# Kernel tuning notes

Measured on AMD Instinct MI355X. Metric: run time of the kernel, lower is better.

Reference implementation:

```python
import jax, jax.numpy as jnp
import numpy as np

N_NODES = 100000
N_EDGES = 1600000
IN_DIM = 128
HID_DIM = 32
OUT_DIM = 64
N_REL = 8
N_CLASSES = 2


def setup_inputs() -> dict:
    key = jax.random.key(0)
    ks = jax.random.split(key, 12)
    x = jax.random.normal(ks[0], (N_NODES, IN_DIM), dtype=jnp.float32)
    edge_index = jax.random.randint(ks[1], (2, N_EDGES), 0, N_NODES, dtype=jnp.int64)
    edge_type = jax.random.randint(ks[2], (N_EDGES,), 0, N_REL, dtype=jnp.int64)
    # FastRGCNConv params: per-relation weight W [R, in, out], root weight, bias
    def glorot(k, shape):
        fan_in, fan_out = shape[-2], shape[-1]
        s = jnp.sqrt(6.0 / (fan_in + fan_out))
        return jax.random.uniform(k, shape, jnp.float32, -s, s)
    W1 = glorot(ks[3], (N_REL, IN_DIM, HID_DIM))
    root1 = glorot(ks[4], (IN_DIM, HID_DIM))
    b1 = jnp.zeros((HID_DIM,), jnp.float32)
    W2 = glorot(ks[5], (N_REL, HID_DIM, OUT_DIM))
    root2 = glorot(ks[6], (HID_DIM, OUT_DIM))
    b2 = jnp.zeros((OUT_DIM,), jnp.float32)
    lin_w = glorot(ks[7], (OUT_DIM, N_CLASSES))
    lin_b = jnp.zeros((N_CLASSES,), jnp.float32)
    return {"x": x, "edge_index": edge_index, "edge_type": edge_type,
            "W1": W1, "root1": root1, "b1": b1,
            "W2": W2, "root2": root2, "b2": b2,
            "lin_w": lin_w, "lin_b": lin_b}


def _fast_rgcn_conv(x, W, root, b, src, dst, etype, n_nodes):
    """FastRGCNConv: per-relation transform, gather by (src, relation),
    mean-aggregate by destination, plus root transform and bias."""
    # Transform all nodes by all relation weights: [N, R, H]
    xW = jnp.einsum('nf,rfh->nrh', x, W)
    # Per-edge message: relation-specific transformed source feature [E, H]
    msg = xW[src, etype]
    agg = jax.ops.segment_sum(msg, dst, num_segments=n_nodes)
    deg = jax.ops.segment_sum(jnp.ones((src.shape[0],), x.dtype), dst,
                              num_segments=n_nodes)
    agg = agg / jnp.maximum(deg, 1.0)[:, None]  # mean aggregation
    return agg + x @ root + b


def reference(x, edge_index, edge_type, W1, root1, b1, W2, root2, b2, lin_w, lin_b):
    src, dst = edge_index[0], edge_index[1]
    n = x.shape[0]
    h = jax.nn.relu(_fast_rgcn_conv(x, W1, root1, b1, src, dst, edge_type, n))
    h = _fast_rgcn_conv(h, W2, root2, b2, src, dst, edge_type, n)
    return h @ lin_w + lin_b
```

## Files before the change

### kernel.cpp

```cpp
#include <hip/hip_runtime.h>

#define NN      100000
#define IN_DIM  128
#define HID     32
#define ODIM    64
#define L1C     288
#define L2K     288
#define NWGS    196
#define NCB     784
#define CCAP    40
#define RECCAP  2304
#define G2ST    296
#define PKCAP   512

using bf16x8 = __attribute__((ext_vector_type(8))) short;
using f32x4  = __attribute__((ext_vector_type(4))) float;

__device__ __forceinline__ float bf2f(short s) {
    unsigned int u = ((unsigned int)(unsigned short)s) << 16;
    float f; __builtin_memcpy(&f, &u, 4); return f;
}
__device__ __forceinline__ short f2bf(float f) {
    unsigned int u; __builtin_memcpy(&u, &f, 4);
    u += 0x7fffu + ((u >> 16) & 1u);
    return (short)(u >> 16);
}
__device__ __forceinline__ float ldf(const void* p, int i, int f32) {
    return f32 ? ((const float*)p)[i] : bf2f(((const short*)p)[i]);
}
__device__ __forceinline__ int ldi(const int* p, long long i, int i64) {
    return i64 ? p[2 * i] : p[(int)i];
}

__global__ __launch_bounds__(1024) void detect(const short* __restrict__ x,
                                               const short* __restrict__ W1,
                                               const short* __restrict__ r1,
                                               const short* __restrict__ W2,
                                               const short* __restrict__ r2,
                                               const short* __restrict__ lw,
                                               const int* __restrict__ ei,
                                               const int* __restrict__ et,
                                               int* __restrict__ flags) {
    __shared__ int cnt[8];
    if (threadIdx.x < 8) cnt[threadIdx.x] = 0;
    __syncthreads();
    const short* ptrs[6] = {x, W1, r1, W2, r2, lw};
    const int    nsmp[6] = {1024, 1024, 1024, 1024, 1024, 64};
    int t = threadIdx.x;
#pragma unroll
    for (int j = 0; j < 6; ++j) {
        if (t < nsmp[j]) {
            unsigned int s = (unsigned short)ptrs[j][2 * t];
            unsigned int e = (s >> 7) & 0xFF;
            if (e >= 140u || (e >= 1u && e <= 100u)) atomicAdd(&cnt[j], 1);
        }
    }
    if (t < 128) {
        if (ei[2 * t + 1] != 0) atomicAdd(&cnt[6], 1);
        if (et[2 * t + 1] != 0) atomicAdd(&cnt[7], 1);
    }
    __syncthreads();
    if (t == 0) {
        const int ns[6] = {1024, 1024, 1024, 1024, 1024, 64};
        for (int j = 0; j < 6; ++j) flags[j] = (cnt[j] * 4 > ns[j]) ? 1 : 0;
        flags[6] = (cnt[6] == 0) ? 1 : 0;
        flags[7] = (cnt[7] == 0) ? 1 : 0;
    }
}

__global__ __launch_bounds__(256) void prep_all(const void* __restrict__ W1,
                                                const void* __restrict__ root1,
                                                const void* __restrict__ W2,
                                                const void* __restrict__ root2,
                                                const short* __restrict__ b1,
                                                const short* __restrict__ b2,
                                                const void* __restrict__ lin_w,
                                                const short* __restrict__ lin_b,
                                                short* __restrict__ w1t,
                                                short* __restrict__ w2ct,
                                                short* __restrict__ smallc,
                                                int* __restrict__ cbTot,
                                                const int* __restrict__ flags) {
    if (blockIdx.x == 0) {
        for (int j = threadIdx.x; j < NCB; j += 256) cbTot[j] = 0;
    }
    int gi = blockIdx.x * 256 + threadIdx.x;
    if (gi < L1C * IN_DIM) {
        int c = gi >> 7, f = gi & 127;
        float v;
        if (c < 256) { int r = c >> 5, h = c & 31; v = ldf(W1, (r * IN_DIM + f) * HID + h, flags[1]); }
        else         { v = ldf(root1, f * HID + (c - 256), flags[2]); }
        w1t[c * IN_DIM + f] = f2bf(v);
        return;
    }
    int i2 = gi - L1C * IN_DIM;
    if (i2 < ODIM * L2K) {
        int c = i2 / L2K, k = i2 % L2K;
        float v;
        if (k < 256) { int r = k >> 5, kk = k & 31; v = ldf(W2, (r * HID + kk) * ODIM + c, flags[3]); }
        else         { v = ldf(root2, (k - 256) * ODIM + c, flags[4]); }
        w2ct[c * L2K + k] = f2bf(v);
        return;
    }
    int i3 = i2 - ODIM * L2K;
    if (i3 < 256) {
        if (i3 < 32)        smallc[i3] = b1[i3];
        else if (i3 < 96)   smallc[i3] = b2[i3 - 32];
        else if (i3 < 224)  smallc[i3] = f2bf(ldf(lin_w, i3 - 96, flags[5]));
        else if (i3 < 226)  smallc[i3] = lin_b[i3 - 224];
    }
}

__global__ __launch_bounds__(1024) void scatter_coarse(const int* __restrict__ ei,
                                                       const int* __restrict__ et,
                                                       int* __restrict__ cnt,
                                                       int* __restrict__ cbTot,
                                                       int* __restrict__ seg, int E,
                                                       const int* __restrict__ flags) {
    __shared__ int cur[NCB];
    if (threadIdx.x < NCB) cur[threadIdx.x] = 0;
    __syncthreads();
    int i64 = flags[6], t64 = flags[7];
    int epw = (E + NWGS - 1) / NWGS;
    int lo = blockIdx.x * epw;
    int hi = lo + epw; if (hi > E) hi = E;
    for (int i = lo + threadIdx.x; i < hi; i += 1024) {
        int s = ldi(ei, i, i64);
        int d = ldi(ei, (long long)E + i, i64);
        int r = ldi(et, i, t64);
        int cb = d >> 7;
        int pos = atomicAdd(&cur[cb], 1);
        if (pos < CCAP)
            seg[(cb * NWGS + (int)blockIdx.x) * CCAP + pos] = ((d & 127) << 20) | (s << 3) | r;
    }
    __syncthreads();
    if (threadIdx.x < NCB) {
        int c = cur[threadIdx.x];
        c = c < CCAP ? c : CCAP;
        cnt[blockIdx.x * NCB + threadIdx.x] = c;
        atomicAdd(&cbTot[threadIdx.x], c);
    }
}

__global__ __launch_bounds__(256) void build_cb(const int* __restrict__ cnt,
                                                const int* __restrict__ seg,
                                                const int* __restrict__ cbTot,
                                                int* __restrict__ off,
                                                float* __restrict__ inv_deg,
                                                int* __restrict__ packed) {
    __shared__ int cntl[NWGS], soff[NWGS];
    __shared__ int recs[RECCAP];
    __shared__ int deg8[1024], base8[1024], kcur8[1024];
    __shared__ int stmp[256];
    __shared__ int gbase_s;
    int cb = blockIdx.x, tid = threadIdx.x;
    {
        int part = 0;
        for (int j = tid; j < cb; j += 256) part += cbTot[j];
        stmp[tid] = part; __syncthreads();
        for (int o = 128; o > 0; o >>= 1) {
            if (tid < o) stmp[tid] += stmp[tid + o];
            __syncthreads();
        }
        if (tid == 0) gbase_s = stmp[0];
        __syncthreads();
    }
    if (tid < NWGS) cntl[tid] = cnt[tid * NCB + cb];
#pragma unroll
    for (int j = 0; j < 4; ++j) { deg8[tid + j * 256] = 0; kcur8[tid + j * 256] = 0; }
    __syncthreads();
    int v = (tid < NWGS) ? cntl[tid] : 0;
    stmp[tid] = v; __syncthreads();
    for (int o = 1; o < 256; o <<= 1) {
        int u = (tid >= o) ? stmp[tid - o] : 0;
        __syncthreads();
        stmp[tid] += u;
        __syncthreads();
    }
    if (tid < NWGS) soff[tid] = stmp[tid] - v;
    int tot = stmp[255]; if (tot > RECCAP) tot = RECCAP;
    __syncthreads();
    int wave = tid >> 6, lane = tid & 63;
    for (int g = wave; g < NWGS; g += 4) {
        int c = cntl[g], b = soff[g];
        const int* sp = seg + (cb * NWGS + g) * CCAP;
        for (int e = lane; e < c; e += 64)
            if (b + e < RECCAP) recs[b + e] = sp[e];
    }
    __syncthreads();
    for (int i = tid; i < tot; i += 256) {
        int rec = recs[i];
        atomicAdd(&deg8[((rec >> 20) << 3) | (rec & 7)], 1);
    }
    __syncthreads();
    int k0 = tid * 4;
    int d0 = deg8[k0], d1 = deg8[k0 + 1], d2 = deg8[k0 + 2], d3 = deg8[k0 + 3];
    int s01 = d0 + d1, sum4 = s01 + d2 + d3;
    stmp[tid] = sum4; __syncthreads();
    for (int o = 1; o < 256; o <<= 1) {
        int u = (tid >= o) ? stmp[tid - o] : 0;
        __syncthreads();
        stmp[tid] += u;
        __syncthreads();
    }
    int excl = stmp[tid] - sum4;
    base8[k0] = excl; base8[k0 + 1] = excl + d0;
    base8[k0 + 2] = excl + s01; base8[k0 + 3] = excl + s01 + d2;
    __syncthreads();
    int gbase = gbase_s;
    if (tid < 128) {
        int b0 = base8[tid * 8];
        int b1 = (tid < 127) ? base8[(tid + 1) * 8] : tot;
        int dv = b1 - b0;
        int node = cb * 128 + tid;
        if (node <= NN) {
            off[node] = gbase + b0;
            if (node < NN) inv_deg[node] = 1.0f / (float)(dv > 1 ? dv : 1);
        }
    }
    __syncthreads();
    for (int i = tid; i < tot; i += 256) {
        int rec = recs[i];
        int key = ((rec >> 20) << 3) | (rec & 7);
        int p = atomicAdd(&kcur8[key], 1);
        packed[gbase + base8[key] + p] = (((rec >> 20) & 15) << 24) | (rec & 0xFFFFF);
    }
}

__global__ __launch_bounds__(256) void gemm1(const void* __restrict__ x,
                                             const short* __restrict__ w1t,
                                             short* __restrict__ xw,
                                             const int* __restrict__ flags) {
    int wave = threadIdx.x >> 6, lane = threadIdx.x & 63;
    int m = lane & 15, quad = lane >> 4;
    int row0 = (blockIdx.x * 4 + wave) * 64;
    if (row0 >= NN) return;

    bf16x8 a[4][4];
    int fp32 = flags[0];
#pragma unroll
    for (int t = 0; t < 4; ++t) {
        int row = row0 + t * 16 + m;
        int rc = row < NN ? row : NN - 1;
        if (fp32) {
            const float* xr = (const float*)x + rc * IN_DIM + quad * 8;
#pragma unroll
            for (int kt = 0; kt < 4; ++kt) {
                const f32x4* q = (const f32x4*)(xr + kt * 32);
                f32x4 u0 = q[0], u1 = q[1];
                bf16x8 tt;
                tt[0] = f2bf(u0[0]); tt[1] = f2bf(u0[1]); tt[2] = f2bf(u0[2]); tt[3] = f2bf(u0[3]);
                tt[4] = f2bf(u1[0]); tt[5] = f2bf(u1[1]); tt[6] = f2bf(u1[2]); tt[7] = f2bf(u1[3]);
                a[t][kt] = tt;
            }
        } else {
            const short* xr = (const short*)x + rc * IN_DIM + quad * 8;
#pragma unroll
            for (int kt = 0; kt < 4; ++kt) a[t][kt] = *(const bf16x8*)(xr + kt * 32);
        }
    }

    for (int ct = 0; ct < 18; ++ct) {
        const short* wp = w1t + (ct * 16 + m) * IN_DIM + quad * 8;
        bf16x8 b[4];
#pragma unroll
        for (int kt = 0; kt < 4; ++kt) b[kt] = *(const bf16x8*)(wp + kt * 32);
#pragma unroll
        for (int t = 0; t < 4; ++t) {
            f32x4 acc = {0.f, 0.f, 0.f, 0.f};
#pragma unroll
            for (int kt = 0; kt < 4; ++kt)
                acc = __builtin_amdgcn_mfma_f32_16x16x32_bf16(a[t][kt], b[kt], acc, 0, 0, 0);
#pragma unroll
            for (int i = 0; i < 4; ++i) {
                int r = row0 + t * 16 + quad * 4 + i;
                if (r < NN) xw[r * L1C + ct * 16 + m] = f2bf(acc[i]);
            }
        }
    }
}

__global__ __launch_bounds__(256) void agg1(const short* __restrict__ xw,
                                            const int* __restrict__ off,
                                            const int* __restrict__ packed,
                                            const float* __restrict__ inv_deg,
                                            const short* __restrict__ smallc,
                                            short* __restrict__ h) {
    __shared__ int pk_l[PKCAP];
    __shared__ float invl[16];
    int tid = threadIdx.x;
    int row0 = blockIdx.x * 16;
    if (tid < 16) invl[tid] = inv_deg[row0 + tid];
    int st = off[row0];
    int tot = off[row0 + 16] - st;
    for (int j = tid; j < tot && j < PKCAP; j += 256) pk_l[j] = packed[st + j];
    __syncthreads();

    int node = tid >> 4, l = tid & 15;
    int s = off[row0 + node] - st, en = off[row0 + node + 1] - st;
    const short* xp = xw + l * 2;
    float a0 = 0.f, a1 = 0.f;

    auto ldpk = [&](int j) -> int {
        return (j < PKCAP) ? pk_l[j] : packed[st + j];
    };
    auto gv = [&](int pk) -> unsigned {
        return *(const unsigned*)(xp + ((pk >> 3) & 0x1FFFF) * L1C + (pk & 7) * 32);
    };

    int i = s;
    for (; i + 7 < en; i += 8) {
        int p0 = ldpk(i),     p1 = ldpk(i + 1), p2 = ldpk(i + 2), p3 = ldpk(i + 3);
        int p4 = ldpk(i + 4), p5 = ldpk(i + 5), p6 = ldpk(i + 6), p7 = ldpk(i + 7);
        unsigned v0 = gv(p0), v1 = gv(p1), v2 = gv(p2), v3 = gv(p3);
        unsigned v4 = gv(p4), v5 = gv(p5), v6 = gv(p6), v7 = gv(p7);
        a0 += ((bf2f((short)(v0 & 0xFFFF)) + bf2f((short)(v1 & 0xFFFF)))
             + (bf2f((short)(v2 & 0xFFFF)) + bf2f((short)(v3 & 0xFFFF))))
            + ((bf2f((short)(v4 & 0xFFFF)) + bf2f((short)(v5 & 0xFFFF)))
             + (bf2f((short)(v6 & 0xFFFF)) + bf2f((short)(v7 & 0xFFFF))));
        a1 += ((bf2f((short)(v0 >> 16)) + bf2f((short)(v1 >> 16)))
             + (bf2f((short)(v2 >> 16)) + bf2f((short)(v3 >> 16))))
            + ((bf2f((short)(v4 >> 16)) + bf2f((short)(v5 >> 16)))
             + (bf2f((short)(v6 >> 16)) + bf2f((short)(v7 >> 16))));
    }
    for (; i + 3 < en; i += 4) {
        int p0 = ldpk(i), p1 = ldpk(i + 1), p2 = ldpk(i + 2), p3 = ldpk(i + 3);
        unsigned v0 = gv(p0), v1 = gv(p1), v2 = gv(p2), v3 = gv(p3);
        a0 += (bf2f((short)(v0 & 0xFFFF)) + bf2f((short)(v1 & 0xFFFF)))
            + (bf2f((short)(v2 & 0xFFFF)) + bf2f((short)(v3 & 0xFFFF)));
        a1 += (bf2f((short)(v0 >> 16)) + bf2f((short)(v1 >> 16)))
            + (bf2f((short)(v2 >> 16)) + bf2f((short)(v3 >> 16)));
    }
    for (; i < en; ++i) {
        unsigned v = gv(ldpk(i));
        a0 += bf2f((short)(v & 0xFFFF));
        a1 += bf2f((short)(v >> 16));
    }

    float inv = invl[node];
    unsigned rt = *(const unsigned*)(xw + (row0 + node) * L1C + 256 + l * 2);
    unsigned bc = *(const unsigned*)(smallc + l * 2);
    float o0 = a0 * inv + bf2f((short)(rt & 0xFFFF)) + bf2f((short)(bc & 0xFFFF));
    float o1 = a1 * inv + bf2f((short)(rt >> 16)) + bf2f((short)(bc >> 16));
    o0 = o0 > 0.f ? o0 : 0.f;
    o1 = o1 > 0.f ? o1 : 0.f;
    unsigned w = ((unsigned)(unsigned short)f2bf(o1) << 16) | (unsigned short)f2bf(o0);
    *(unsigned*)(h + (row0 + node) * HID + l * 2) = w;
}

__global__ __launch_bounds__(256) void agg2_fused(const short* __restrict__ h,
                                                  const int* __restrict__ off,
                                                  const int* __restrict__ packed,
                                                  const float* __restrict__ inv_deg,
                                                  const short* __restrict__ w2ct,
                                                  const short* __restrict__ smallc,
                                                  float* __restrict__ out) {
    __shared__ __align__(16) short g2l[16 * G2ST];
    __shared__ int pk_l[PKCAP];
    __shared__ float red[4][16][2];
    __shared__ float invl[16];
    int tid = threadIdx.x;
    int row0 = blockIdx.x * 16;
    if (tid < 16) invl[tid] = inv_deg[row0 + tid];
    int st = off[row0];
    int tot = off[row0 + 16] - st;
    {
        unsigned* gz = (unsigned*)g2l;
        const int nu = 16 * G2ST / 2;
        for (int j = tid; j < nu; j += 256) gz[j] = 0;
        for (int j = tid; j < tot && j < PKCAP; j += 256) pk_l[j] = packed[st + j];
    }
    __syncthreads();

    int node = tid >> 4, l = tid & 15;
    int s = off[row0 + node] - st, en = off[row0 + node + 1] - st;
    float inv = invl[node];
    const short* hp = h + l * 2;
    short* grow = g2l + node * G2ST + l * 2;
    float a0 = 0.f, a1 = 0.f;
    int cur = -1;

    auto ldpk = [&](int j) -> int {
        return (j < PKCAP) ? pk_l[j] : packed[st + j];
    };
    auto acc_edge = [&](int pk, unsigned hv) {
        int rel = pk & 7;
        bool nr = (rel != cur);
        float lo = bf2f((short)(hv & 0xFFFF)) * inv;
        float hi = bf2f((short)(hv >> 16)) * inv;
        a0 = (nr ? 0.f : a0) + lo;
        a1 = (nr ? 0.f : a1) + hi;
        cur = rel;
        unsigned w = ((unsigned)(unsigned short)f2bf(a1) << 16)
                   | (unsigned short)f2bf(a0);
        *(unsigned*)(grow + rel * 32) = w;
    };

    int i = s;
    for (; i + 7 < en; i += 8) {
        int p0 = ldpk(i),     p1 = ldpk(i + 1), p2 = ldpk(i + 2), p3 = ldpk(i + 3);
        int p4 = ldpk(i + 4), p5 = ldpk(i + 5), p6 = ldpk(i + 6), p7 = ldpk(i + 7);
        unsigned v0 = *(const unsigned*)(hp + ((p0 >> 3) & 0x1FFFF) * HID);
        unsigned v1 = *(const unsigned*)(hp + ((p1 >> 3) & 0x1FFFF) * HID);
        unsigned v2 = *(const unsigned*)(hp + ((p2 >> 3) & 0x1FFFF) * HID);
        unsigned v3 = *(const unsigned*)(hp + ((p3 >> 3) & 0x1FFFF) * HID);
        unsigned v4 = *(const unsigned*)(hp + ((p4 >> 3) & 0x1FFFF) * HID);
        unsigned v5 = *(const unsigned*)(hp + ((p5 >> 3) & 0x1FFFF) * HID);
        unsigned v6 = *(const unsigned*)(hp + ((p6 >> 3) & 0x1FFFF) * HID);
        unsigned v7 = *(const unsigned*)(hp + ((p7 >> 3) & 0x1FFFF) * HID);
        acc_edge(p0, v0); acc_edge(p1, v1); acc_edge(p2, v2); acc_edge(p3, v3);
        acc_edge(p4, v4); acc_edge(p5, v5); acc_edge(p6, v6); acc_edge(p7, v7);
    }
    for (; i + 3 < en; i += 4) {
        int p0 = ldpk(i), p1 = ldpk(i + 1), p2 = ldpk(i + 2), p3 = ldpk(i + 3);
        unsigned v0 = *(const unsigned*)(hp + ((p0 >> 3) & 0x1FFFF) * HID);
        unsigned v1 = *(const unsigned*)(hp + ((p1 >> 3) & 0x1FFFF) * HID);
        unsigned v2 = *(const unsigned*)(hp + ((p2 >> 3) & 0x1FFFF) * HID);
        unsigned v3 = *(const unsigned*)(hp + ((p3 >> 3) & 0x1FFFF) * HID);
        acc_edge(p0, v0); acc_edge(p1, v1); acc_edge(p2, v2); acc_edge(p3, v3);
    }
    for (; i < en; ++i) {
        int p = ldpk(i);
        unsigned v = *(const unsigned*)(hp + ((p >> 3) & 0x1FFFF) * HID);
        acc_edge(p, v);
    }

    *(unsigned*)(grow + 256) = *(const unsigned*)(h + (row0 + node) * HID + l * 2);
    __syncthreads();

    int wave = tid >> 6, lane = tid & 63;
    int m15 = lane & 15, quad = lane >> 4;
    const short* wp = w2ct + (wave * 16 + m15) * L2K + quad * 8;
    bf16x8 a[9], b[9];
#pragma unroll
    for (int kt = 0; kt < 9; ++kt) {
        b[kt] = *(const bf16x8*)(wp + kt * 32);
        a[kt] = *(const bf16x8*)(&g2l[m15 * G2ST + quad * 8 + kt * 32]);
    }
    f32x4 acc = {0.f, 0.f, 0.f, 0.f};
#pragma unroll
    for (int kt = 0; kt < 9; ++kt)
        acc = __builtin_amdgcn_mfma_f32_16x16x32_bf16(a[kt], b[kt], acc, 0, 0, 0);

    int c = wave * 16 + m15;
    float lw0 = bf2f(smallc[96 + c * 2 + 0]);
    float lw1 = bf2f(smallc[96 + c * 2 + 1]);
    float b2c = bf2f(smallc[32 + c]);
    float pr0[4], pr1[4];
#pragma unroll
    for (int i2 = 0; i2 < 4; ++i2) {
        float v = acc[i2] + b2c;
        pr0[i2] = v * lw0;
        pr1[i2] = v * lw1;
    }
#pragma unroll
    for (int o = 1; o < 16; o <<= 1) {
#pragma unroll
        for (int i2 = 0; i2 < 4; ++i2) {
            pr0[i2] += __shfl_xor(pr0[i2], o, 64);
            pr1[i2] += __shfl_xor(pr1[i2], o, 64);
        }
    }
    if (m15 == 0) {
#pragma unroll
        for (int i2 = 0; i2 < 4; ++i2) {
            red[wave][quad * 4 + i2][0] = pr0[i2];
            red[wave][quad * 4 + i2][1] = pr1[i2];
        }
    }
    __syncthreads();
    if (tid < 32) {
        int row = tid >> 1, j = tid & 1;
        float v = red[0][row][j] + red[1][row][j] + red[2][row][j] + red[3][row][j]
                + bf2f(smallc[224 + j]);
        out[(row0 + row) * 2 + j] = v;
    }
}

extern "C" void kernel_launch(void* const* d_in, const int* in_sizes, int n_in,
                              void* d_out, int out_size, void* d_ws, size_t ws_size,
                              hipStream_t stream) {
    const void* x     = d_in[0];
    const int*  ei    = (const int*)d_in[1];
    const int*  etype = (const int*)d_in[2];
    const void* W1    = d_in[3];
    const void* root1 = d_in[4];
    const void* b1    = d_in[5];
    const void* W2    = d_in[6];
    const void* root2 = d_in[7];
    const void* b2    = d_in[8];
    const void* lin_w = d_in[9];
    const void* lin_b = d_in[10];
    float* out = (float*)d_out;

    const int E = in_sizes[2];

    char* p = (char*)d_ws;
    auto alloc = [&](size_t bytes) { char* r = p; p += (bytes + 255) & ~(size_t)255; return (void*)r; };
    int*   flags   = (int*)  alloc(256);
    int*   off     = (int*)  alloc((size_t)(NN + 1) * 4);
    float* inv_deg = (float*)alloc((size_t)NN * 4);
    int*   packed  = (int*)  alloc((size_t)E * 4);
    int*   cnt     = (int*)  alloc((size_t)NWGS * NCB * 4);
    int*   cbTot   = (int*)  alloc((size_t)NCB * 4);
    int*   seg     = (int*)  alloc((size_t)NCB * NWGS * CCAP * 4);
    short* w1t     = (short*)alloc((size_t)L1C * IN_DIM * 2);
    short* w2ct    = (short*)alloc((size_t)ODIM * L2K * 2);
    short* smallc  = (short*)alloc(256 * 2);
    short* h       = (short*)alloc((size_t)NN * HID * 2);
    short* xw1     = (short*)alloc((size_t)NN * L1C * 2);

    detect<<<1, 1024, 0, stream>>>((const short*)x, (const short*)W1, (const short*)root1,
                                   (const short*)W2, (const short*)root2, (const short*)lin_w,
                                   ei, etype, flags);
    const int prep_items = L1C * IN_DIM + ODIM * L2K + 256;
    prep_all<<<(prep_items + 255) / 256, 256, 0, stream>>>(W1, root1, W2, root2,
                                                           (const short*)b1, (const short*)b2,
                                                           lin_w, (const short*)lin_b,
                                                           w1t, w2ct, smallc, cbTot, flags);

    scatter_coarse<<<NWGS, 1024, 0, stream>>>(ei, etype, cnt, cbTot, seg, E, flags);
    build_cb<<<NCB, 256, 0, stream>>>(cnt, seg, cbTot, off, inv_deg, packed);

    gemm1<<<((NN + 63) / 64 + 3) / 4, 256, 0, stream>>>(x, w1t, xw1, flags);
    agg1<<<NN / 16, 256, 0, stream>>>(xw1, off, packed, inv_deg, smallc, h);
    agg2_fused<<<NN / 16, 256, 0, stream>>>(h, off, packed, inv_deg, w2ct, smallc, out);
}
```

Baseline: 280.3 us.

## Aggregate raw features per relation before layer-1 GEMM and fuse into one kernel

Result: slower. 335.9 us (+19.8%).

```diff
diff --git a/kernel.cpp b/kernel.cpp
--- a/kernel.cpp
+++ b/kernel.cpp
@@ -5,12 +5,14 @@
 #define HID     32
 #define ODIM    64
 #define L1C     288
+#define L1K     1152
 #define L2K     288
 #define NWGS    196
 #define NCB     784
 #define CCAP    40
 #define RECCAP  2304
 #define G2ST    296
+#define SST     1160
 #define PKCAP   512
 
 using bf16x8 = __attribute__((ext_vector_type(8))) short;
@@ -76,7 +78,7 @@
                                                 const short* __restrict__ b2,
                                                 const void* __restrict__ lin_w,
                                                 const short* __restrict__ lin_b,
-                                                short* __restrict__ w1t,
+                                                short* __restrict__ w1tn,
                                                 short* __restrict__ w2ct,
                                                 short* __restrict__ smallc,
                                                 int* __restrict__ cbTot,
@@ -85,15 +87,15 @@
         for (int j = threadIdx.x; j < NCB; j += 256) cbTot[j] = 0;
     }
     int gi = blockIdx.x * 256 + threadIdx.x;
-    if (gi < L1C * IN_DIM) {
-        int c = gi >> 7, f = gi & 127;
+    if (gi < HID * L1K) {
+        int c = gi / L1K, k = gi - c * L1K;
         float v;
-        if (c < 256) { int r = c >> 5, h = c & 31; v = ldf(W1, (r * IN_DIM + f) * HID + h, flags[1]); }
-        else         { v = ldf(root1, f * HID + (c - 256), flags[2]); }
-        w1t[c * IN_DIM + f] = f2bf(v);
+        if (k < 1024) { int r = k >> 7, f = k & 127; v = ldf(W1, (r * IN_DIM + f) * HID + c, flags[1]); }
+        else          { v = ldf(root1, (k - 1024) * HID + c, flags[2]); }
+        w1tn[c * L1K + k] = f2bf(v);
         return;
     }
-    int i2 = gi - L1C * IN_DIM;
+    int i2 = gi - HID * L1K;
     if (i2 < ODIM * L2K) {
         int c = i2 / L2K, k = i2 % L2K;
         float v;
@@ -108,6 +110,22 @@
         else if (i3 < 96)   smallc[i3] = b2[i3 - 32];
         else if (i3 < 224)  smallc[i3] = f2bf(ldf(lin_w, i3 - 96, flags[5]));
         else if (i3 < 226)  smallc[i3] = lin_b[i3 - 224];
+    }
+}
+
+__global__ __launch_bounds__(256) void xcast(const void* __restrict__ x,
+                                             short* __restrict__ xb,
+                                             const int* __restrict__ flags) {
+    int gi = blockIdx.x * 256 + threadIdx.x;
+    if (flags[0]) {
+        const f32x4* q = (const f32x4*)x + gi * 2;
+        f32x4 u0 = q[0], u1 = q[1];
+        bf16x8 t;
+        t[0] = f2bf(u0[0]); t[1] = f2bf(u0[1]); t[2] = f2bf(u0[2]); t[3] = f2bf(u0[3]);
+        t[4] = f2bf(u1[0]); t[5] = f2bf(u1[1]); t[6] = f2bf(u1[2]); t[7] = f2bf(u1[3]);
+        ((bf16x8*)xb)[gi] = t;
+    } else {
+        ((bf16x8*)xb)[gi] = ((const bf16x8*)x)[gi];
     }
 }
 
@@ -227,125 +245,100 @@
     }
 }
 
-__global__ __launch_bounds__(256) void gemm1(const void* __restrict__ x,
-                                             const short* __restrict__ w1t,
-                                             short* __restrict__ xw,
-                                             const int* __restrict__ flags) {
-    int wave = threadIdx.x >> 6, lane = threadIdx.x & 63;
-    int m = lane & 15, quad = lane >> 4;
-    int row0 = (blockIdx.x * 4 + wave) * 64;
-    if (row0 >= NN) return;
-
-    bf16x8 a[4][4];
-    int fp32 = flags[0];
-#pragma unroll
-    for (int t = 0; t < 4; ++t) {
-        int row = row0 + t * 16 + m;
-        int rc = row < NN ? row : NN - 1;
-        if (fp32) {
-            const float* xr = (const float*)x + rc * IN_DIM + quad * 8;
-#pragma unroll
-            for (int kt = 0; kt < 4; ++kt) {
-                const f32x4* q = (const f32x4*)(xr + kt * 32);
-                f32x4 u0 = q[0], u1 = q[1];
-                bf16x8 tt;
-                tt[0] = f2bf(u0[0]); tt[1] = f2bf(u0[1]); tt[2] = f2bf(u0[2]); tt[3] = f2bf(u0[3]);
-                tt[4] = f2bf(u1[0]); tt[5] = f2bf(u1[1]); tt[6] = f2bf(u1[2]); tt[7] = f2bf(u1[3]);
-                a[t][kt] = tt;
-            }
-        } else {
-            const short* xr = (const short*)x + rc * IN_DIM + quad * 8;
-#pragma unroll
-            for (int kt = 0; kt < 4; ++kt) a[t][kt] = *(const bf16x8*)(xr + kt * 32);
-        }
-    }
-
-    for (int ct = 0; ct < 18; ++ct) {
-        const short* wp = w1t + (ct * 16 + m) * IN_DIM + quad * 8;
-        bf16x8 b[4];
-#pragma unroll
-        for (int kt = 0; kt < 4; ++kt) b[kt] = *(const bf16x8*)(wp + kt * 32);
-#pragma unroll
-        for (int t = 0; t < 4; ++t) {
-            f32x4 acc = {0.f, 0.f, 0.f, 0.f};
-#pragma unroll
-            for (int kt = 0; kt < 4; ++kt)
-                acc = __builtin_amdgcn_mfma_f32_16x16x32_bf16(a[t][kt], b[kt], acc, 0, 0, 0);
-#pragma unroll
-            for (int i = 0; i < 4; ++i) {
-                int r = row0 + t * 16 + quad * 4 + i;
-                if (r < NN) xw[r * L1C + ct * 16 + m] = f2bf(acc[i]);
-            }
-        }
-    }
-}
-
-__global__ __launch_bounds__(256) void agg1(const short* __restrict__ xw,
-                                            const int* __restrict__ off,
-                                            const int* __restrict__ packed,
-                                            const float* __restrict__ inv_deg,
-                                            const short* __restrict__ smallc,
-                                            short* __restrict__ h) {
-    __shared__ int pk_l[PKCAP];
+__global__ __launch_bounds__(256) void agg_gemm1(const short* __restrict__ xb,
+                                                 const int* __restrict__ off,
+                                                 const int* __restrict__ packed,
+                                                 const float* __restrict__ inv_deg,
+                                                 const short* __restrict__ w1tn,
+                                                 const short* __restrict__ smallc,
+                                                 short* __restrict__ h) {
+    __shared__ __align__(16) short S[16 * SST];
+    __shared__ __align__(16) int pk_l[PKCAP];
     __shared__ float invl[16];
+    float* red2 = (float*)pk_l;
     int tid = threadIdx.x;
     int row0 = blockIdx.x * 16;
     if (tid < 16) invl[tid] = inv_deg[row0 + tid];
     int st = off[row0];
     int tot = off[row0 + 16] - st;
-    for (int j = tid; j < tot && j < PKCAP; j += 256) pk_l[j] = packed[st + j];
+    {
+        uint4 z = {0, 0, 0, 0};
+        uint4* sz = (uint4*)S;
+        for (int j = tid; j < 16 * SST / 8; j += 256) sz[j] = z;
+        for (int j = tid; j < tot && j < PKCAP; j += 256) pk_l[j] = packed[st + j];
+    }
     __syncthreads();
 
     int node = tid >> 4, l = tid & 15;
     int s = off[row0 + node] - st, en = off[row0 + node + 1] - st;
-    const short* xp = xw + l * 2;
-    float a0 = 0.f, a1 = 0.f;
-
-    auto ldpk = [&](int j) -> int {
-        return (j < PKCAP) ? pk_l[j] : packed[st + j];
+    float inv = invl[node];
+    const short* xp = xb + l * 8;
+    short* Sp = S + node * SST + l * 8;
+    float ac[8] = {0.f, 0.f, 0.f, 0.f, 0.f, 0.f, 0.f, 0.f};
+    int cur = -1;
+
+    auto acc_edge = [&](int pk, bf16x8 v) {
+        int rel = pk & 7;
+        bool nr = (rel != cur);
+        bf16x8 wv;
+#pragma unroll
+        for (int d = 0; d < 8; ++d) {
+            float xv = bf2f(v[d]);
+            ac[d] = (nr ? 0.f : ac[d]) + xv * inv;
+            wv[d] = f2bf(ac[d]);
+        }
+        cur = rel;
+        *(bf16x8*)(Sp + rel * 128) = wv;
     };
-    auto gv = [&](int pk) -> unsigned {
-        return *(const unsigned*)(xp + ((pk >> 3) & 0x1FFFF) * L1C + (pk & 7) * 32);
+    auto run = [&](auto LD) {
+        int i = s;
+        for (; i + 3 < en; i += 4) {
+            int p0 = LD(i), p1 = LD(i + 1), p2 = LD(i + 2), p3 = LD(i + 3);
+            bf16x8 v0 = *(const bf16x8*)(xp + ((p0 >> 3) & 0x1FFFF) * IN_DIM);
+            bf16x8 v1 = *(const bf16x8*)(xp + ((p1 >> 3) & 0x1FFFF) * IN_DIM);
+            bf16x8 v2 = *(const bf16x8*)(xp + ((p2 >> 3) & 0x1FFFF) * IN_DIM);
+            bf16x8 v3 = *(const bf16x8*)(xp + ((p3 >> 3) & 0x1FFFF) * IN_DIM);
+            acc_edge(p0, v0); acc_edge(p1, v1); acc_edge(p2, v2); acc_edge(p3, v3);
+        }
+        for (; i < en; ++i) {
+            int p = LD(i);
+            bf16x8 v = *(const bf16x8*)(xp + ((p >> 3) & 0x1FFFF) * IN_DIM);
+            acc_edge(p, v);
+        }
     };
-
-    int i = s;
-    for (; i + 7 < en; i += 8) {
-        int p0 = ldpk(i),     p1 = ldpk(i + 1), p2 = ldpk(i + 2), p3 = ldpk(i + 3);
-        int p4 = ldpk(i + 4), p5 = ldpk(i + 5), p6 = ldpk(i + 6), p7 = ldpk(i + 7);
-        unsigned v0 = gv(p0), v1 = gv(p1), v2 = gv(p2), v3 = gv(p3);
-        unsigned v4 = gv(p4), v5 = gv(p5), v6 = gv(p6), v7 = gv(p7);
-        a0 += ((bf2f((short)(v0 & 0xFFFF)) + bf2f((short)(v1 & 0xFFFF)))
-             + (bf2f((short)(v2 & 0xFFFF)) + bf2f((short)(v3 & 0xFFFF))))
-            + ((bf2f((short)(v4 & 0xFFFF)) + bf2f((short)(v5 & 0xFFFF)))
-             + (bf2f((short)(v6 & 0xFFFF)) + bf2f((short)(v7 & 0xFFFF))));
-        a1 += ((bf2f((short)(v0 >> 16)) + bf2f((short)(v1 >> 16)))
-             + (bf2f((short)(v2 >> 16)) + bf2f((short)(v3 >> 16))))
-            + ((bf2f((short)(v4 >> 16)) + bf2f((short)(v5 >> 16)))
-             + (bf2f((short)(v6 >> 16)) + bf2f((short)(v7 >> 16))));
-    }
-    for (; i + 3 < en; i += 4) {
-        int p0 = ldpk(i), p1 = ldpk(i + 1), p2 = ldpk(i + 2), p3 = ldpk(i + 3);
-        unsigned v0 = gv(p0), v1 = gv(p1), v2 = gv(p2), v3 = gv(p3);
-        a0 += (bf2f((short)(v0 & 0xFFFF)) + bf2f((short)(v1 & 0xFFFF)))
-            + (bf2f((short)(v2 & 0xFFFF)) + bf2f((short)(v3 & 0xFFFF)));
-        a1 += (bf2f((short)(v0 >> 16)) + bf2f((short)(v1 >> 16)))
-            + (bf2f((short)(v2 >> 16)) + bf2f((short)(v3 >> 16)));
-    }
-    for (; i < en; ++i) {
-        unsigned v = gv(ldpk(i));
-        a0 += bf2f((short)(v & 0xFFFF));
-        a1 += bf2f((short)(v >> 16));
-    }
-
-    float inv = invl[node];
-    unsigned rt = *(const unsigned*)(xw + (row0 + node) * L1C + 256 + l * 2);
-    unsigned bc = *(const unsigned*)(smallc + l * 2);
-    float o0 = a0 * inv + bf2f((short)(rt & 0xFFFF)) + bf2f((short)(bc & 0xFFFF));
-    float o1 = a1 * inv + bf2f((short)(rt >> 16)) + bf2f((short)(bc >> 16));
-    o0 = o0 > 0.f ? o0 : 0.f;
-    o1 = o1 > 0.f ? o1 : 0.f;
-    unsigned w = ((unsigned)(unsigned short)f2bf(o1) << 16) | (unsigned short)f2bf(o0);
-    *(unsigned*)(h + (row0 + node) * HID + l * 2) = w;
+    if (tot <= PKCAP) run([&](int j) { return pk_l[j]; });
+    else              run([&](int j) { return (j < PKCAP) ? pk_l[j] : packed[st + j]; });
+
+    *(bf16x8*)(Sp + 1024) = *(const bf16x8*)(xb + (row0 + node) * IN_DIM + l * 8);
+    __syncthreads();
+
+    int wave = tid >> 6, lane = tid & 63;
+    int m15 = lane & 15, quad = lane >> 4;
+    int ct2 = wave & 1, kh = wave >> 1;
+    const short* wp = w1tn + (ct2 * 16 + m15) * L1K + kh * 576 + quad * 8;
+    const short* ap = S + m15 * SST + kh * 576 + quad * 8;
+    f32x4 acc = {0.f, 0.f, 0.f, 0.f};
+    for (int ks = 0; ks < 18; ++ks) {
+        bf16x8 b = *(const bf16x8*)(wp + ks * 32);
+        bf16x8 a = *(const bf16x8*)(ap + ks * 32);
+        acc = __builtin_amdgcn_mfma_f32_16x16x32_bf16(a, b, acc, 0, 0, 0);
+    }
+    if (wave >= 2) {
+#pragma unroll
+        for (int i2 = 0; i2 < 4; ++i2)
+            red2[ct2 * 256 + (quad * 4 + i2) * 16 + m15] = acc[i2];
+    }
+    __syncthreads();
+    if (wave < 2) {
+        int c = ct2 * 16 + m15;
+        float bias = bf2f(smallc[c]);
+#pragma unroll
+        for (int i2 = 0; i2 < 4; ++i2) {
+            float o = acc[i2] + red2[ct2 * 256 + (quad * 4 + i2) * 16 + m15] + bias;
+            o = o > 0.f ? o : 0.f;
+            h[(row0 + quad * 4 + i2) * HID + c] = f2bf(o);
+        }
+    }
 }
 
 __global__ __launch_bounds__(256) void agg2_fused(const short* __restrict__ h,
@@ -504,25 +497,25 @@
     int*   cnt     = (int*)  alloc((size_t)NWGS * NCB * 4);
     int*   cbTot   = (int*)  alloc((size_t)NCB * 4);
     int*   seg     = (int*)  alloc((size_t)NCB * NWGS * CCAP * 4);
-    short* w1t     = (short*)alloc((size_t)L1C * IN_DIM * 2);
+    short* w1tn    = (short*)alloc((size_t)HID * L1K * 2);
     short* w2ct    = (short*)alloc((size_t)ODIM * L2K * 2);
     short* smallc  = (short*)alloc(256 * 2);
     short* h       = (short*)alloc((size_t)NN * HID * 2);
-    short* xw1     = (short*)alloc((size_t)NN * L1C * 2);
+    short* xb      = (short*)alloc((size_t)NN * IN_DIM * 2);
 
     detect<<<1, 1024, 0, stream>>>((const short*)x, (const short*)W1, (const short*)root1,
                                    (const short*)W2, (const short*)root2, (const short*)lin_w,
                                    ei, etype, flags);
-    const int prep_items = L1C * IN_DIM + ODIM * L2K + 256;
+    const int prep_items = HID * L1K + ODIM * L2K + 256;
     prep_all<<<(prep_items + 255) / 256, 256, 0, stream>>>(W1, root1, W2, root2,
                                                            (const short*)b1, (const short*)b2,
                                                            lin_w, (const short*)lin_b,
-                                                           w1t, w2ct, smallc, cbTot, flags);
+                                                           w1tn, w2ct, smallc, cbTot, flags);
+    xcast<<<NN * IN_DIM / 8 / 256, 256, 0, stream>>>(x, xb, flags);
 
     scatter_coarse<<<NWGS, 1024, 0, stream>>>(ei, etype, cnt, cbTot, seg, E, flags);
     build_cb<<<NCB, 256, 0, stream>>>(cnt, seg, cbTot, off, inv_deg, packed);
 
-    gemm1<<<((NN + 63) / 64 + 3) / 4, 256, 0, stream>>>(x, w1t, xw1, flags);
-    agg1<<<NN / 16, 256, 0, stream>>>(xw1, off, packed, inv_deg, smallc, h);
+    agg_gemm1<<<NN / 16, 256, 0, stream>>>(xb, off, packed, inv_deg, w1tn, smallc, h);
     agg2_fused<<<NN / 16, 256, 0, stream>>>(h, off, packed, inv_deg, w2ct, smallc, out);
 }
```
